# Optimization experiments

Hardware: AMD Instinct MI355X
Metric: run time of the kernel (lower is better)

Reference implementation:

```python
import jax, jax.numpy as jnp
import numpy as np

NUM_HEAD = 16
SIZE_PER_HEAD = 64
D_MODEL = NUM_HEAD * SIZE_PER_HEAD
BATCH = 4
SEQ = 2048
MASK_VAL = 1e10  # module uses 10000000000.0 for the causal mask


def setup_inputs() -> dict:
    key = jax.random.key(0)
    ks = jax.random.split(key, 11)
    s = 1.0 / np.sqrt(D_MODEL)
    return {
        "q": jax.random.normal(ks[0], (BATCH, SEQ, D_MODEL), jnp.float32),
        "k": jax.random.normal(ks[1], (BATCH, SEQ, D_MODEL), jnp.float32),
        "v": jax.random.normal(ks[2], (BATCH, SEQ, D_MODEL), jnp.float32),
        "WQ": jax.random.normal(ks[3], (D_MODEL, D_MODEL), jnp.float32) * s,
        "WQ_bias": jax.random.normal(ks[4], (D_MODEL,), jnp.float32) * 0.02,
        "WK": jax.random.normal(ks[5], (D_MODEL, D_MODEL), jnp.float32) * s,
        "WK_bias": jax.random.normal(ks[6], (D_MODEL,), jnp.float32) * 0.02,
        "WV": jax.random.normal(ks[7], (D_MODEL, D_MODEL), jnp.float32) * s,
        "WV_bias": jax.random.normal(ks[8], (D_MODEL,), jnp.float32) * 0.02,
        "WO": jax.random.normal(ks[9], (D_MODEL, D_MODEL), jnp.float32) * s,
        "WO_bias": jax.random.normal(ks[10], (D_MODEL,), jnp.float32) * 0.02,
    }


def _split_heads(x):
    # [B, S, H*D] -> [B, H, S, D]
    b, s, _ = x.shape
    return x.reshape(b, s, NUM_HEAD, SIZE_PER_HEAD).transpose(0, 2, 1, 3)


def reference(q, k, v, WQ, WQ_bias, WK, WK_bias, WV, WV_bias, WO, WO_bias):
    Q = _split_heads(q @ WQ + WQ_bias)  # [B,H,M,D]
    Kh = _split_heads(k @ WK + WK_bias)  # [B,H,N,D]
    Vh = _split_heads(v @ WV + WV_bias)  # [B,H,N,D]

    A = jnp.einsum('bhmd,bhnd->bhmn', Q, Kh)
    # causal mask (is_right=True): subtract 1e10 on strict upper triangle,
    # applied BEFORE the 1/sqrt(d) scale, exactly as the original.
    m, n = A.shape[-2], A.shape[-1]
    causal = jnp.triu(jnp.ones((m, n), A.dtype), k=1) * jnp.asarray(MASK_VAL, A.dtype)
    A = A - causal
    A = jax.nn.softmax(A / np.sqrt(SIZE_PER_HEAD).astype(np.float32), axis=-1)

    O = jnp.einsum('bhmn,bhnd->bhmd', A, Vh)  # [B,H,M,D]
    b, h, s, d = O.shape
    O = O.transpose(0, 2, 1, 3).reshape(b, s, h * d)
    return O @ WO + WO_bias
```

## Files before the change

kernel.cpp:

```cpp
#include <hip/hip_runtime.h>
#include <hip/hip_bf16.h>

typedef unsigned short u16;
typedef __attribute__((ext_vector_type(8))) short bf8_t;
typedef __attribute__((ext_vector_type(4))) float f4_t;
typedef __attribute__((ext_vector_type(2))) unsigned u32x2_t;
typedef __attribute__((ext_vector_type(4))) unsigned u32x4_t;

#define D_MODEL 1024
#define SEQ     2048
#define NHEAD   16
#define DH      64
#define MTOK    8192
#define ELEMS_PER_MAT 8388608

__device__ __forceinline__ u16 f2b(float x) {
    unsigned u = __float_as_uint(x);
    u += 0x7fffu + ((u >> 16) & 1u);
    return (u16)(u >> 16);
}

__device__ __forceinline__ unsigned pkrn(float lo, float hi) {
    __hip_bfloat162 h = __float22bfloat162_rn(make_float2(lo, hi));
    unsigned r;
    __builtin_memcpy(&r, &h, 4);
    return r;
}

__device__ __forceinline__ float ex2(float x) {
    float r;
    asm("v_exp_f32 %0, %1" : "=v"(r) : "v"(x));
    return r;
}

__device__ __forceinline__ void gl_lds16(const void* g, void* l) {
    __builtin_amdgcn_global_load_lds(
        (const __attribute__((address_space(1))) void*)g,
        (__attribute__((address_space(3))) void*)l, 16, 0, 0);
}

struct P3 { const float* p[3]; };
__global__ void cvt_in3(P3 src, u16* __restrict__ dst) {
    int z = blockIdx.y;
    const float* s = src.p[z];
    u16* d = dst + (size_t)z * ELEMS_PER_MAT;
    int i = blockIdx.x * 256 + threadIdx.x;
    const float4* s4 = (const float4*)s;
    float4 a = s4[i * 2];
    float4 b = s4[i * 2 + 1];
    bf8_t o;
    o[0] = (short)f2b(a.x); o[1] = (short)f2b(a.y);
    o[2] = (short)f2b(a.z); o[3] = (short)f2b(a.w);
    o[4] = (short)f2b(b.x); o[5] = (short)f2b(b.y);
    o[6] = (short)f2b(b.z); o[7] = (short)f2b(b.w);
    *(bf8_t*)&d[(size_t)i * 8] = o;
}

#define QSCALE 0.1803368801111244f
struct W4 { const float* w[4]; };
__global__ void cvt_wt(W4 wa, u16* __restrict__ wt) {
    int z = blockIdx.z;
    const float* W = wa.w[z];
    u16* Wt = wt + (size_t)z * 1048576;
    float scale = (z == 0) ? QSCALE : 1.0f;
    __shared__ float tl[64][65];
    int t = threadIdx.x;
    int bx = blockIdx.x, by = blockIdx.y;
#pragma unroll
    for (int i = 0; i < 16; i++) {
        int e = i * 256 + t;
        int row = e >> 6, col = e & 63;
        tl[row][col] = W[(size_t)(by * 64 + row) * 1024 + bx * 64 + col];
    }
    __syncthreads();
#pragma unroll
    for (int i = 0; i < 16; i++) {
        int e = i * 256 + t;
        int row = e >> 6, col = e & 63;
        Wt[(size_t)(bx * 64 + row) * 1024 + by * 64 + col] = f2b(tl[col][row] * scale);
    }
}

struct B4 { const float* b[4]; };
__global__ void cvt_bias(B4 ba, float* __restrict__ dst) {
    int t = threadIdx.x;
    for (int z = 0; z < 4; z++) {
        float sc = (z == 0) ? QSCALE : 1.0f;
        for (int i = t; i < 1024; i += 256) dst[z * 1024 + i] = ba.b[z][i] * sc;
    }
}

template <int MODE>
__global__ __launch_bounds__(256, 2) void gemm_k(const u16* __restrict__ Ab,
                                                 const u16* __restrict__ Btb,
                                                 const float* __restrict__ biasb,
                                                 void* __restrict__ out0,
                                                 u16* __restrict__ outV) {
    int z = blockIdx.z;
    const u16* A  = Ab  + (size_t)z * ELEMS_PER_MAT;
    const u16* Bt = Btb + (size_t)z * 1048576;
    const float* bias = biasb + z * 1024;
    bool vswap = (MODE == 3) && (z == 2);

    int bid = blockIdx.y * 64 + blockIdx.x;
    int xcd = bid & 7, seq = bid >> 3;
    int tm = xcd * 8 + (seq & 7);
    int tn = seq >> 3;
    int t = threadIdx.x;
    int wid = t >> 6, lane = t & 63;
    int wm = wid >> 1, wn = wid & 1;
    int la = lane & 15, lh = lane >> 4;

    __shared__ __align__(16) char smem[65536];

    f4_t acc[4][4];
#pragma unroll
    for (int m = 0; m < 4; m++)
#pragma unroll
        for (int n = 0; n < 4; n++) acc[m][n] = (f4_t){0.f, 0.f, 0.f, 0.f};

    const u16* Agb = A  + (size_t)(tm * 128) * 1024;
    const u16* Bgb = Bt + (size_t)(tn * 128) * 1024;

    int ch0 = wid * 64 + lane;
    int so0 = (lh ^ (la & 7)) * 8;
    int so1 = so0 ^ 32;

    auto stage = [&](int k0, int b) {
#pragma unroll
        for (int i = 0; i < 4; i++) {
            int ch = ch0 + i * 256;
            int row = ch >> 3, c8 = ch & 7;
            int srcc = (c8 ^ (row & 7)) * 8;
            gl_lds16(Agb + (size_t)row * 1024 + k0 + srcc,
                     smem + b * 32768 + (size_t)(i * 4 + wid) * 1024);
            gl_lds16(Bgb + (size_t)row * 1024 + k0 + srcc,
                     smem + b * 32768 + 16384 + (size_t)(i * 4 + wid) * 1024);
        }
    };

    stage(0, 0);
    __syncthreads();
    int cur = 0;
    for (int kt = 0; kt < 16; kt++) {
        if (kt + 1 < 16) stage((kt + 1) * 64, cur ^ 1);
        const u16* As = (const u16*)(smem + cur * 32768);
        const u16* Bs = (const u16*)(smem + cur * 32768 + 16384);
#pragma unroll
        for (int ks = 0; ks < 2; ks++) {
            int so = ks ? so1 : so0;
            bf8_t af[4], bf[4];
#pragma unroll
            for (int m = 0; m < 4; m++)
                af[m] = *(const bf8_t*)&As[(wm * 64 + m * 16 + la) * 64 + so];
#pragma unroll
            for (int n = 0; n < 4; n++)
                bf[n] = *(const bf8_t*)&Bs[(wn * 64 + n * 16 + la) * 64 + so];
            if (vswap) {
#pragma unroll
                for (int m = 0; m < 4; m++)
#pragma unroll
                    for (int n = 0; n < 4; n++)
                        acc[m][n] = __builtin_amdgcn_mfma_f32_16x16x32_bf16(bf[n], af[m], acc[m][n], 0, 0, 0);
            } else {
#pragma unroll
                for (int m = 0; m < 4; m++)
#pragma unroll
                    for (int n = 0; n < 4; n++)
                        acc[m][n] = __builtin_amdgcn_mfma_f32_16x16x32_bf16(af[m], bf[n], acc[m][n], 0, 0, 0);
            }
        }
        __syncthreads();
        cur ^= 1;
    }

    int lh4 = lh * 4;
    int bq = tm >> 4;
    int sloc = (tm & 15) * 128;

    if (MODE == 1) {
        float* ef = (float*)smem;
#pragma unroll
        for (int m = 0; m < 4; m++) {
            int row = wm * 64 + m * 16 + lh4;
#pragma unroll
            for (int n = 0; n < 4; n++) {
                int cb = wn * 64 + n * 16;
                float bv = bias[tn * 128 + cb + la];
#pragma unroll
                for (int r = 0; r < 4; r++)
                    ef[(row + r) * 128 + cb + la] = acc[m][n][r] + bv;
            }
        }
        __syncthreads();
        float* og = (float*)out0;
#pragma unroll
        for (int p = 0; p < 16; p++) {
            int e = t * 4 + p * 1024;
            int row = e >> 7, col = e & 127;
            f4_t v = *(const f4_t*)&ef[e];
            *(f4_t*)&og[(size_t)(tm * 128 + row) * 1024 + tn * 128 + col] = v;
        }
    } else if (vswap) {
        u16* eb = (u16*)smem;
#pragma unroll
        for (int m = 0; m < 4; m++) {
            int s = wm * 64 + m * 16 + la;
#pragma unroll
            for (int n = 0; n < 4; n++) {
                int cb = wn * 64 + n * 16 + lh4;
#pragma unroll
                for (int r = 0; r < 4; r++)
                    eb[(cb + r) * 128 + s] = f2b(acc[m][n][r] + bias[tn * 128 + cb + r]);
            }
        }
        __syncthreads();
#pragma unroll
        for (int p = 0; p < 8; p++) {
            int col = (t >> 4) + p * 16;
            int chunk = (t & 15) * 8;
            int h = tn * 2 + (col >> 6), d = col & 63;
            bf8_t v = *(const bf8_t*)&eb[col * 128 + chunk];
            *(bf8_t*)&outV[(((size_t)(bq * NHEAD + h)) * DH + d) * SEQ + sloc + chunk] = v;
        }
    } else {
        u16* eb = (u16*)smem;
#pragma unroll
        for (int m = 0; m < 4; m++) {
            int row = wm * 64 + m * 16 + lh4;
#pragma unroll
            for (int n = 0; n < 4; n++) {
                int cb = wn * 64 + n * 16;
                float bv = bias[tn * 128 + cb + la];
#pragma unroll
                for (int r = 0; r < 4; r++)
                    eb[wn * 8192 + (row + r) * 64 + n * 16 + la] = f2b(acc[m][n][r] + bv);
            }
        }
        __syncthreads();
        u16* outz = (u16*)out0 + (size_t)z * ELEMS_PER_MAT;
        size_t gbase = ((size_t)(bq * NHEAD + tn * 2) * SEQ + sloc) * DH;
#pragma unroll
        for (int p = 0; p < 8; p++) {
            int e = t * 8 + p * 2048;
            int hl = e >> 13, inner = e & 8191;
            bf8_t v = *(const bf8_t*)&eb[e];
            *(bf8_t*)&outz[gbase + (size_t)hl * SEQ * DH + inner] = v;
        }
    }
}

__global__ __launch_bounds__(256, 4) void attn(const u16* __restrict__ Qp,
                                               const u16* __restrict__ Kp,
                                               const u16* __restrict__ Vt,
                                               u16* __restrict__ ctx) {
    int id = blockIdx.x;
    int qt = 31 - (id >> 6);
    int bh = id & 63;
    int t = threadIdx.x, wid = t >> 6, lane = t & 63;
    int la = lane & 15, lh = lane >> 4;
    int lh4 = lh * 4;
    int lh8 = lh * 8;
    int q0 = qt * 64;

    const u16* Qb = Qp + (size_t)bh * SEQ * DH;
    const u16* Kb = Kp + (size_t)bh * SEQ * DH;
    const u16* Vb = Vt + (size_t)bh * DH * SEQ;

    __shared__ __align__(16) u16 Kl[2 * 4096];
    __shared__ __align__(16) u16 Vl[2 * 4096];

    int qrow = q0 + wid * 16 + la;
    bf8_t qf0 = *(const bf8_t*)&Qb[(size_t)qrow * DH + lh8];
    bf8_t qf1 = *(const bf8_t*)&Qb[(size_t)qrow * DH + 32 + lh8];

    bf8_t onesf;
#pragma unroll
    for (int i = 0; i < 8; i++) onesf[i] = (short)0x3F80;

    f4_t o[4] = {};
    f4_t o5  = {};

    int s0 = t, s1 = t + 256;
    int rr0 = s0 >> 3, rr1 = s1 >> 3;
    int ck0 = ((s0 & 7) ^ (rr0 & 7)) * 8;
    int ck1 = ((s1 & 7) ^ (rr1 & 7)) * 8;
    int key0 = (rr0 & 0x23) | ((rr0 & 0x0C) << 1) | ((rr0 & 0x10) >> 2);
    int key1 = (rr1 & 0x23) | ((rr1 & 0x0C) << 1) | ((rr1 & 0x10) >> 2);
    const u16* kp0 = Kb + (size_t)key0 * DH + ck0;
    const u16* kp1 = Kb + (size_t)key1 * DH + ck1;
    const u16* vp0 = Vb + (size_t)rr0 * SEQ + ck0;
    const u16* vp1 = Vb + (size_t)rr1 * SEQ + ck1;

    int ntiles = qt + 1;
    auto stage = [&](int tile, int b) {
        int kv0 = tile * 64;
        gl_lds16(kp0 + (size_t)kv0 * DH, (char*)Kl + b * 8192 + wid * 1024);
        gl_lds16(kp1 + (size_t)kv0 * DH, (char*)Kl + b * 8192 + 4096 + wid * 1024);
        gl_lds16(vp0 + kv0,              (char*)Vl + b * 8192 + wid * 1024);
        gl_lds16(vp1 + kv0,              (char*)Vl + b * 8192 + 4096 + wid * 1024);
    };
    stage(0, 0);

    int csA = (lh ^ (la & 7)) * 8;
    int csB = ((4 | lh) ^ (la & 7)) * 8;

    for (int tkv = 0; tkv < ntiles; ++tkv) {
        __syncthreads();
        if (tkv + 1 < ntiles) stage(tkv + 1, (tkv + 1) & 1);
        const u16* Kd = Kl + (tkv & 1) * 4096;
        const u16* Vd = Vl + (tkv & 1) * 4096;

        bool diag = (tkv == qt);
        int ntmax = diag ? ((wid < 2) ? 2 : 4) : 4;

        f4_t st[4];
        __builtin_amdgcn_s_setprio(1);
#pragma unroll
        for (int nt = 0; nt < 4; nt++) {
            if (nt < ntmax) {
                bf8_t kf0 = *(const bf8_t*)&Kd[(nt * 16 + la) * 64 + csA];
                bf8_t kf1 = *(const bf8_t*)&Kd[(nt * 16 + la) * 64 + csB];
                f4_t a = (f4_t){0.f, 0.f, 0.f, 0.f};
                a = __builtin_amdgcn_mfma_f32_16x16x32_bf16(kf0, qf0, a, 0, 0, 0);
                a = __builtin_amdgcn_mfma_f32_16x16x32_bf16(kf1, qf1, a, 0, 0, 0);
                if (diag) {
                    int kbase = ((nt >> 1) << 5) + (lh << 3) + ((nt & 1) << 2);
#pragma unroll
                    for (int r = 0; r < 4; r++)
                        if (kbase + r > wid * 16 + la) a[r] = -1e30f;
                }
                st[nt] = a;
            } else {
                st[nt] = (f4_t){-1e30f, -1e30f, -1e30f, -1e30f};
            }
        }
        __builtin_amdgcn_s_setprio(0);

#pragma unroll
        for (int nt = 0; nt < 4; nt++) {
#pragma unroll
            for (int r = 0; r < 4; r++)
                st[nt][r] = ex2(st[nt][r]);
        }

        __builtin_amdgcn_s_setprio(1);
#pragma unroll
        for (int kk = 0; kk < 2; kk++) {
            if (2 * kk < ntmax) {
                u32x4_t pw;
                pw[0] = pkrn(st[2 * kk][0], st[2 * kk][1]);
                pw[1] = pkrn(st[2 * kk][2], st[2 * kk][3]);
                pw[2] = pkrn(st[2 * kk + 1][0], st[2 * kk + 1][1]);
                pw[3] = pkrn(st[2 * kk + 1][2], st[2 * kk + 1][3]);
                bf8_t pf;
                __builtin_memcpy(&pf, &pw, 16);
                int cs = kk ? csB : csA;
#pragma unroll
                for (int dm = 0; dm < 4; dm++) {
                    bf8_t vf = *(const bf8_t*)&Vd[(dm * 16 + la) * 64 + cs];
                    o[dm] = __builtin_amdgcn_mfma_f32_16x16x32_bf16(vf, pf, o[dm], 0, 0, 0);
                }
                o5 = __builtin_amdgcn_mfma_f32_16x16x32_bf16(onesf, pf, o5, 0, 0, 0);
            }
        }
        __builtin_amdgcn_s_setprio(0);
    }

    float inv = 1.0f / o5[0];
    int b = bh >> 4, h = bh & 15;
    size_t base = ((size_t)(b * SEQ + qrow)) * D_MODEL + h * DH;
#pragma unroll
    for (int dm = 0; dm < 4; dm++) {
        u32x2_t w;
        w[0] = pkrn(o[dm][0] * inv, o[dm][1] * inv);
        w[1] = pkrn(o[dm][2] * inv, o[dm][3] * inv);
        *(u32x2_t*)&ctx[base + dm * 16 + lh4] = w;
    }
}

extern "C" void kernel_launch(void* const* d_in, const int* in_sizes, int n_in,
                              void* d_out, int out_size, void* d_ws, size_t ws_size,
                              hipStream_t stream) {
    const float* q   = (const float*)d_in[0];
    const float* k   = (const float*)d_in[1];
    const float* v   = (const float*)d_in[2];
    const float* WQ  = (const float*)d_in[3];
    const float* WQb = (const float*)d_in[4];
    const float* WK  = (const float*)d_in[5];
    const float* WKb = (const float*)d_in[6];
    const float* WV  = (const float*)d_in[7];
    const float* WVb = (const float*)d_in[8];
    const float* WO  = (const float*)d_in[9];
    const float* WOb = (const float*)d_in[10];

    char* ws = (char*)d_ws;
    u16*   qkv_bf = (u16*)(ws);
    u16*   Wt     = (u16*)(ws + 50331648);
    float* biasws = (float*)(ws + 58720256);
    u16*   QKVp   = (u16*)(ws + 58736640);
    u16*   Vt_    = (u16*)(ws + 109068288);
    u16*   ctx    = (u16*)(ws + 125845504);

    P3 p3; p3.p[0] = q; p3.p[1] = k; p3.p[2] = v;
    cvt_in3<<<dim3(4096, 3), 256, 0, stream>>>(p3, qkv_bf);

    W4 w4; w4.w[0] = WQ; w4.w[1] = WK; w4.w[2] = WV; w4.w[3] = WO;
    cvt_wt<<<dim3(16, 16, 4), 256, 0, stream>>>(w4, Wt);
    B4 b4; b4.b[0] = WQb; b4.b[1] = WKb; b4.b[2] = WVb; b4.b[3] = WOb;
    cvt_bias<<<1, 256, 0, stream>>>(b4, biasws);

    gemm_k<3><<<dim3(64, 8, 3), 256, 0, stream>>>(qkv_bf, Wt, biasws, QKVp, Vt_);

    attn<<<dim3(2048), 256, 0, stream>>>(QKVp, QKVp + ELEMS_PER_MAT, Vt_, ctx);

    gemm_k<1><<<dim3(64, 8, 1), 256, 0, stream>>>(ctx, Wt + 3 * 1048576,
                                                  biasws + 3 * 1024, d_out, nullptr);
}
```

Measured before the change: 172.9 us.

## Process 128 query rows per attention block to reuse staged K/V tiles

Each attention block now handles a 128-row query tile, with every wave owning two 16-row groups, instead of a 64-row tile. Each K/V tile staged into LDS and each K/V fragment read from LDS now feeds twice the MFMA work, so global and LDS traffic per unit of compute drops. The grid halves to 1024 blocks, and causal skipping is done per 16-row group. The cost is more accumulator registers per thread, fewer blocks to balance the triangular workload, and less occupancy.

```diff
diff --git a/kernel.cpp b/kernel.cpp
--- a/kernel.cpp
+++ b/kernel.cpp
@@ -255,13 +255,12 @@
                                                const u16* __restrict__ Vt,
                                                u16* __restrict__ ctx) {
     int id = blockIdx.x;
-    int qt = 31 - (id >> 6);
+    int qt = 15 - (id >> 6);
     int bh = id & 63;
     int t = threadIdx.x, wid = t >> 6, lane = t & 63;
     int la = lane & 15, lh = lane >> 4;
-    int lh4 = lh * 4;
-    int lh8 = lh * 8;
-    int q0 = qt * 64;
+    int lh4 = lh * 4, lh8 = lh * 8;
+    int q0 = qt * 128;
 
     const u16* Qb = Qp + (size_t)bh * SEQ * DH;
     const u16* Kb = Kp + (size_t)bh * SEQ * DH;
@@ -270,16 +269,19 @@
     __shared__ __align__(16) u16 Kl[2 * 4096];
     __shared__ __align__(16) u16 Vl[2 * 4096];
 
-    int qrow = q0 + wid * 16 + la;
-    bf8_t qf0 = *(const bf8_t*)&Qb[(size_t)qrow * DH + lh8];
-    bf8_t qf1 = *(const bf8_t*)&Qb[(size_t)qrow * DH + 32 + lh8];
+    int qr0 = q0 + wid * 32 + la;
+    int qr1 = qr0 + 16;
+    bf8_t qf00 = *(const bf8_t*)&Qb[(size_t)qr0 * DH + lh8];
+    bf8_t qf01 = *(const bf8_t*)&Qb[(size_t)qr0 * DH + 32 + lh8];
+    bf8_t qf10 = *(const bf8_t*)&Qb[(size_t)qr1 * DH + lh8];
+    bf8_t qf11 = *(const bf8_t*)&Qb[(size_t)qr1 * DH + 32 + lh8];
 
     bf8_t onesf;
 #pragma unroll
     for (int i = 0; i < 8; i++) onesf[i] = (short)0x3F80;
 
-    f4_t o[4] = {};
-    f4_t o5  = {};
+    f4_t o0[4] = {}, o1[4] = {};
+    f4_t l0 = {}, l1 = {};
 
     int s0 = t, s1 = t + 256;
     int rr0 = s0 >> 3, rr1 = s1 >> 3;
@@ -292,7 +294,7 @@
     const u16* vp0 = Vb + (size_t)rr0 * SEQ + ck0;
     const u16* vp1 = Vb + (size_t)rr1 * SEQ + ck1;
 
-    int ntiles = qt + 1;
+    int ntiles = 2 * qt + 2;
     auto stage = [&](int tile, int b) {
         int kv0 = tile * 64;
         gl_lds16(kp0 + (size_t)kv0 * DH, (char*)Kl + b * 8192 + wid * 1024);
@@ -304,6 +306,8 @@
 
     int csA = (lh ^ (la & 7)) * 8;
     int csB = ((4 | lh) ^ (la & 7)) * 8;
+    int qmax0 = q0 + wid * 32 + 15;
+    int qmax1 = qmax0 + 16;
 
     for (int tkv = 0; tkv < ntiles; ++tkv) {
         __syncthreads();
@@ -311,71 +315,98 @@
         const u16* Kd = Kl + (tkv & 1) * 4096;
         const u16* Vd = Vl + (tkv & 1) * 4096;
 
-        bool diag = (tkv == qt);
-        int ntmax = diag ? ((wid < 2) ? 2 : 4) : 4;
-
-        f4_t st[4];
+        bool diag = (tkv >= ntiles - 2);
+        int kt64 = tkv * 64;
+
+        u32x4_t pp0[2], pp1[2];
+#pragma unroll
+        for (int kk = 0; kk < 2; kk++) {
+            f4_t sA0, sA1, sB0, sB1;
+            __builtin_amdgcn_s_setprio(1);
+#pragma unroll
+            for (int j = 0; j < 2; j++) {
+                int nt = 2 * kk + j;
+                int kmin = kt64 + 32 * kk + 4 * j;
+                bool need0 = kmin <= qmax0;
+                bool need1 = kmin <= qmax1;
+                f4_t a0 = (f4_t){-1e30f, -1e30f, -1e30f, -1e30f};
+                f4_t a1 = a0;
+                if (need0 || need1) {
+                    bf8_t kf0 = *(const bf8_t*)&Kd[(nt * 16 + la) * 64 + csA];
+                    bf8_t kf1 = *(const bf8_t*)&Kd[(nt * 16 + la) * 64 + csB];
+                    if (need0) {
+                        f4_t a = (f4_t){0.f, 0.f, 0.f, 0.f};
+                        a = __builtin_amdgcn_mfma_f32_16x16x32_bf16(kf0, qf00, a, 0, 0, 0);
+                        a = __builtin_amdgcn_mfma_f32_16x16x32_bf16(kf1, qf01, a, 0, 0, 0);
+                        a0 = a;
+                    }
+                    if (need1) {
+                        f4_t a = (f4_t){0.f, 0.f, 0.f, 0.f};
+                        a = __builtin_amdgcn_mfma_f32_16x16x32_bf16(kf0, qf10, a, 0, 0, 0);
+                        a = __builtin_amdgcn_mfma_f32_16x16x32_bf16(kf1, qf11, a, 0, 0, 0);
+                        a1 = a;
+                    }
+                    if (diag) {
+                        int kb = kt64 + 32 * kk + (lh << 3) + 4 * j;
+#pragma unroll
+                        for (int r = 0; r < 4; r++) {
+                            if (kb + r > qr0) a0[r] = -1e30f;
+                            if (kb + r > qr1) a1[r] = -1e30f;
+                        }
+                    }
+                }
+                if (j == 0) { sA0 = a0; sA1 = a1; }
+                else        { sB0 = a0; sB1 = a1; }
+            }
+            __builtin_amdgcn_s_setprio(0);
+            pp0[kk][0] = pkrn(ex2(sA0[0]), ex2(sA0[1]));
+            pp0[kk][1] = pkrn(ex2(sA0[2]), ex2(sA0[3]));
+            pp0[kk][2] = pkrn(ex2(sB0[0]), ex2(sB0[1]));
+            pp0[kk][3] = pkrn(ex2(sB0[2]), ex2(sB0[3]));
+            pp1[kk][0] = pkrn(ex2(sA1[0]), ex2(sA1[1]));
+            pp1[kk][1] = pkrn(ex2(sA1[2]), ex2(sA1[3]));
+            pp1[kk][2] = pkrn(ex2(sB1[0]), ex2(sB1[1]));
+            pp1[kk][3] = pkrn(ex2(sB1[2]), ex2(sB1[3]));
+        }
+
         __builtin_amdgcn_s_setprio(1);
 #pragma unroll
-        for (int nt = 0; nt < 4; nt++) {
-            if (nt < ntmax) {
-                bf8_t kf0 = *(const bf8_t*)&Kd[(nt * 16 + la) * 64 + csA];
-                bf8_t kf1 = *(const bf8_t*)&Kd[(nt * 16 + la) * 64 + csB];
-                f4_t a = (f4_t){0.f, 0.f, 0.f, 0.f};
-                a = __builtin_amdgcn_mfma_f32_16x16x32_bf16(kf0, qf0, a, 0, 0, 0);
-                a = __builtin_amdgcn_mfma_f32_16x16x32_bf16(kf1, qf1, a, 0, 0, 0);
-                if (diag) {
-                    int kbase = ((nt >> 1) << 5) + (lh << 3) + ((nt & 1) << 2);
-#pragma unroll
-                    for (int r = 0; r < 4; r++)
-                        if (kbase + r > wid * 16 + la) a[r] = -1e30f;
-                }
-                st[nt] = a;
-            } else {
-                st[nt] = (f4_t){-1e30f, -1e30f, -1e30f, -1e30f};
-            }
-        }
-        __builtin_amdgcn_s_setprio(0);
-
-#pragma unroll
-        for (int nt = 0; nt < 4; nt++) {
-#pragma unroll
-            for (int r = 0; r < 4; r++)
-                st[nt][r] = ex2(st[nt][r]);
-        }
-
-        __builtin_amdgcn_s_setprio(1);
-#pragma unroll
         for (int kk = 0; kk < 2; kk++) {
-            if (2 * kk < ntmax) {
-                u32x4_t pw;
-                pw[0] = pkrn(st[2 * kk][0], st[2 * kk][1]);
-                pw[1] = pkrn(st[2 * kk][2], st[2 * kk][3]);
-                pw[2] = pkrn(st[2 * kk + 1][0], st[2 * kk + 1][1]);
-                pw[3] = pkrn(st[2 * kk + 1][2], st[2 * kk + 1][3]);
-                bf8_t pf;
-                __builtin_memcpy(&pf, &pw, 16);
+            int kmin = kt64 + 32 * kk;
+            bool n0 = kmin <= qmax0;
+            bool n1 = kmin <= qmax1;
+            if (n0 || n1) {
+                bf8_t pf0, pf1;
+                __builtin_memcpy(&pf0, &pp0[kk], 16);
+                __builtin_memcpy(&pf1, &pp1[kk], 16);
                 int cs = kk ? csB : csA;
 #pragma unroll
                 for (int dm = 0; dm < 4; dm++) {
                     bf8_t vf = *(const bf8_t*)&Vd[(dm * 16 + la) * 64 + cs];
-                    o[dm] = __builtin_amdgcn_mfma_f32_16x16x32_bf16(vf, pf, o[dm], 0, 0, 0);
+                    if (n0) o0[dm] = __builtin_amdgcn_mfma_f32_16x16x32_bf16(vf, pf0, o0[dm], 0, 0, 0);
+                    if (n1) o1[dm] = __builtin_amdgcn_mfma_f32_16x16x32_bf16(vf, pf1, o1[dm], 0, 0, 0);
                 }
-                o5 = __builtin_amdgcn_mfma_f32_16x16x32_bf16(onesf, pf, o5, 0, 0, 0);
+                if (n0) l0 = __builtin_amdgcn_mfma_f32_16x16x32_bf16(onesf, pf0, l0, 0, 0, 0);
+                if (n1) l1 = __builtin_amdgcn_mfma_f32_16x16x32_bf16(onesf, pf1, l1, 0, 0, 0);
             }
         }
         __builtin_amdgcn_s_setprio(0);
     }
 
-    float inv = 1.0f / o5[0];
     int b = bh >> 4, h = bh & 15;
-    size_t base = ((size_t)(b * SEQ + qrow)) * D_MODEL + h * DH;
+    float inv0 = 1.0f / l0[0];
+    float inv1 = 1.0f / l1[0];
+    size_t base0 = ((size_t)(b * SEQ + qr0)) * D_MODEL + h * DH;
+    size_t base1 = ((size_t)(b * SEQ + qr1)) * D_MODEL + h * DH;
 #pragma unroll
     for (int dm = 0; dm < 4; dm++) {
         u32x2_t w;
-        w[0] = pkrn(o[dm][0] * inv, o[dm][1] * inv);
-        w[1] = pkrn(o[dm][2] * inv, o[dm][3] * inv);
-        *(u32x2_t*)&ctx[base + dm * 16 + lh4] = w;
+        w[0] = pkrn(o0[dm][0] * inv0, o0[dm][1] * inv0);
+        w[1] = pkrn(o0[dm][2] * inv0, o0[dm][3] * inv0);
+        *(u32x2_t*)&ctx[base0 + dm * 16 + lh4] = w;
+        w[0] = pkrn(o1[dm][0] * inv1, o1[dm][1] * inv1);
+        w[1] = pkrn(o1[dm][2] * inv1, o1[dm][3] * inv1);
+        *(u32x2_t*)&ctx[base1 + dm * 16 + lh4] = w;
     }
 }
 
@@ -412,7 +443,7 @@
 
     gemm_k<3><<<dim3(64, 8, 3), 256, 0, stream>>>(qkv_bf, Wt, biasws, QKVp, Vt_);
 
-    attn<<<dim3(2048), 256, 0, stream>>>(QKVp, QKVp + ELEMS_PER_MAT, Vt_, ctx);
+    attn<<<dim3(1024), 256, 0, stream>>>(QKVp, QKVp + ELEMS_PER_MAT, Vt_, ctx);
 
     gemm_k<1><<<dim3(64, 8, 1), 256, 0, stream>>>(ctx, Wt + 3 * 1048576,
                                                   biasws + 3 * 1024, d_out, nullptr);
```

New measurement: 185.2 us. 7.1% more time.
